# Kernel tuning notes

Hardware: AMD Instinct MI355X
Metric: run time of the kernel (lower is better)

Reference implementation:

```python
import jax, jax.numpy as jnp
from jax import lax
import numpy as np

B0 = 2          # batch
S = 32          # spatial grid side; L = S*S + 2
L = S * S + 2
DM = 256        # d_model
ED = 512        # d_inner = expand_factor * d_model
N = 16          # d_state
R = 16          # dt_rank = ceil(d_model/16)
K = 4           # d_conv


def _dwconv(x, w, b):
    # x: (B, L, ED) -> causal depthwise conv1d, kernel K, left-pad K-1 (== torch pad K-1 then [:, :, :L])
    xt = jnp.transpose(x, (0, 2, 1))  # (B, ED, L)
    o = lax.conv_general_dilated(xt, w, (1,), [(K - 1, 0)],
                                 feature_group_count=ED,
                                 dimension_numbers=('NCH', 'OIH', 'NCH'))
    return jnp.transpose(o + b[None, :, None], (0, 2, 1))


def _ssm(x, Alog, Dp, xp_w, dt_w, dt_b):
    # x: (B, L, ED); selective scan (mamba.py math, pscan=True path)
    A = -jnp.exp(Alog)                       # (ED, N)
    dBC = x @ xp_w.T                          # (B, L, R+2N)
    delta = jax.nn.softplus(dBC[..., :R] @ dt_w.T + dt_b)  # (B, L, ED)
    Bm = dBC[..., R:R + N]                    # (B, L, N)
    Cm = dBC[..., R + N:]                     # (B, L, N)
    dA = jnp.exp(delta[..., None] * A)        # (B, L, ED, N)
    dBx = (delta * x)[..., None] * Bm[:, :, None, :]  # (B, L, ED, N)

    def comb(e1, e2):
        a1, b1 = e1
        a2, b2 = e2
        return a1 * a2, a2 * b1 + b2

    _, hs = lax.associative_scan(comb, (dA, dBx), axis=1)  # h_t = dA_t*h_{t-1} + dBx_t
    return jnp.einsum('blen,bln->ble', hs, Cm) + Dp * x


def _cross(t):
    # keep first/last token, transpose the SxS interior grid (row-major <-> col-major)
    b, l, d = t.shape
    inner = t[:, 1:-1].reshape(b, S, S, d).transpose(0, 2, 1, 3).reshape(b, S * S, d)
    return jnp.concatenate([t[:, :1], inner, t[:, -1:]], axis=1)


def _branch(xz, cw, cb, xp, dw, db, Al, Dp):
    xa, za = jnp.split(xz, 2, axis=-1)
    xa = jax.nn.silu(_dwconv(xa, cw, cb))
    return _ssm(xa, Al, Dp, xp, dw, db) * jax.nn.silu(za)


def _forward(x, in_w, out_w, *p):
    xz = x @ in_w.T  # (B, L, 2*ED)
    (cwa, cba, xpa, dwa, dba, Ala, Da,
     cwb, cbb, xpb, dwb, dbb, Alb, Db,
     cwc, cbc, xpc, dwc, dbc, Alc, Dc,
     cwd, cbd, xpd, dwd, dbd, Ald, Dd) = p
    ga = _branch(xz, cwa, cba, xpa, dwa, dba, Ala, Da)                # forward scan
    gb = _branch(xz[:, ::-1], cwb, cbb, xpb, dwb, dbb, Alb, Db)       # reversed scan
    xzc = _cross(xz)
    gc = _branch(xzc, cwc, cbc, xpc, dwc, dbc, Alc, Dc)               # transposed scan
    gd = _branch(xzc[:, ::-1], cwd, cbd, xpd, dwd, dbd, Ald, Dd)      # reversed-transposed scan
    # gating commutes with token permutations, so reassemble gated outputs
    y = (ga + gb[:, ::-1] + _cross(gc) + _cross(gd)[:, ::-1]) * 0.25  # divide_output=True
    return y @ out_w.T


def setup_inputs() -> dict:
    keys = jax.random.split(jax.random.key(0), 64)
    it = iter(keys)

    def nrm(shape, scale=0.02):
        return scale * jax.random.normal(next(it), shape, dtype=jnp.float32)

    d = {}
    d['x'] = jax.random.normal(next(it), (B0, L, DM), dtype=jnp.float32)
    d['in_w'] = nrm((2 * ED, DM))
    d['out_w'] = nrm((DM, ED))
    std = R ** -0.5
    for s in ['a', 'b', 'c', 'd']:
        d[f'conv_w_{s}'] = nrm((ED, 1, K), 0.1)
        d[f'conv_b_{s}'] = jnp.zeros((ED,), jnp.float32)
        d[f'xp_w_{s}'] = nrm((R + 2 * N, ED))
        d[f'dt_w_{s}'] = jax.random.uniform(next(it), (ED, R), minval=-std, maxval=std, dtype=jnp.float32)
        dt = jnp.exp(jax.random.uniform(next(it), (ED,), dtype=jnp.float32)
                     * (np.float32(np.log(0.1)) - np.float32(np.log(0.001))) + np.float32(np.log(0.001)))
        d[f'dt_b_{s}'] = dt + jnp.log(-jnp.expm1(-dt))  # inverse-softplus init
        d[f'Alog_{s}'] = jnp.log(jnp.tile(jnp.arange(1, N + 1, dtype=jnp.float32), (ED, 1)))
        d[f'D_{s}'] = jnp.ones((ED,), jnp.float32)
    return d


def reference(x, in_w, out_w,
              conv_w_a, conv_b_a, xp_w_a, dt_w_a, dt_b_a, Alog_a, D_a,
              conv_w_b, conv_b_b, xp_w_b, dt_w_b, dt_b_b, Alog_b, D_b,
              conv_w_c, conv_b_c, xp_w_c, dt_w_c, dt_b_c, Alog_c, D_c,
              conv_w_d, conv_b_d, xp_w_d, dt_w_d, dt_b_d, Alog_d, D_d):
    return _forward(x, in_w, out_w,
                    conv_w_a, conv_b_a, xp_w_a, dt_w_a, dt_b_a, Alog_a, D_a,
                    conv_w_b, conv_b_b, xp_w_b, dt_w_b, dt_b_b, Alog_b, D_b,
                    conv_w_c, conv_b_c, xp_w_c, dt_w_c, dt_b_c, Alog_c, D_c,
                    conv_w_d, conv_b_d, xp_w_d, dt_w_d, dt_b_d, Alog_d, D_d)
```

## Files before the change

kernel.cpp:

```cpp
#include <hip/hip_runtime.h>
#include <math.h>

#define LL 1026
#define EDim 512
#define MM 2052
#define NC 16
#define LC 64

struct Params {
  const float* cw[4];
  const float* cb[4];
  const float* xpw[4];
  const float* dtw[4];
  const float* dtb[4];
  const float* Al[4];
  const float* Dp[4];
};

__device__ __forceinline__ int sigma_map(int branch, int l) {
  if (branch & 1) l = LL - 1 - l;
  if (branch & 2) {
    if (l > 0 && l < LL - 1) {
      int p = l - 1;
      l = 1 + ((p & 31) << 5) + (p >> 5);
    }
  }
  return l;
}

__device__ __forceinline__ float silu_f(float v) {
  return v * __builtin_amdgcn_rcpf(1.f + __expf(-v));
}
__device__ __forceinline__ float softplus_f(float s) {
  return fmaxf(s, 0.f) + __logf(1.f + __expf(-fabsf(s)));
}

template<int CTRL>
__device__ __forceinline__ float dpp_mov0(float x) {
  int r = __builtin_amdgcn_update_dpp(0, __float_as_int(x), CTRL, 0xF, 0xF, false);
  return __int_as_float(r);
}

__device__ __forceinline__ float red16(float r) {
  r += dpp_mov0<0xB1>(r);
  r += dpp_mov0<0x4E>(r);
  r += dpp_mov0<0x114>(r);
  r += dpp_mov0<0x118>(r);
  return r;
}

__global__ __launch_bounds__(256, 2) void k1_gemm_in(
    const float* __restrict__ x, const float* __restrict__ w,
    float* __restrict__ xa, float* __restrict__ sz) {
  __shared__ float As[32][68];
  __shared__ float Bs[32][68];
  const int t = threadIdx.x;
  const int tx = t & 15, ty = t >> 4;
  const int m0 = blockIdx.x * 64, n0 = blockIdx.y * 64;
  float acc[4][4] = {};
  for (int k0 = 0; k0 < 256; k0 += 32) {
    #pragma unroll
    for (int p = 0; p < 2; ++p) {
      int f = t + p * 256;
      int row = f >> 3, cf = f & 7;
      int gr = m0 + row; gr = gr < MM ? gr : MM - 1;
      float4 v = *(const float4*)(x + (size_t)gr * 256 + k0 + cf * 4);
      As[cf*4+0][row] = v.x; As[cf*4+1][row] = v.y;
      As[cf*4+2][row] = v.z; As[cf*4+3][row] = v.w;
      int gn = n0 + row;
      float4 u = *(const float4*)(w + (size_t)gn * 256 + k0 + cf * 4);
      Bs[cf*4+0][row] = u.x; Bs[cf*4+1][row] = u.y;
      Bs[cf*4+2][row] = u.z; Bs[cf*4+3][row] = u.w;
    }
    __syncthreads();
    #pragma unroll
    for (int k = 0; k < 32; ++k) {
      float4 av = *(const float4*)&As[k][ty*4];
      float4 bv = *(const float4*)&Bs[k][tx*4];
      float a0 = av.x, a1 = av.y, a2 = av.z, a3 = av.w;
      float b0 = bv.x, b1 = bv.y, b2 = bv.z, b3 = bv.w;
      acc[0][0]=fmaf(a0,b0,acc[0][0]); acc[0][1]=fmaf(a0,b1,acc[0][1]); acc[0][2]=fmaf(a0,b2,acc[0][2]); acc[0][3]=fmaf(a0,b3,acc[0][3]);
      acc[1][0]=fmaf(a1,b0,acc[1][0]); acc[1][1]=fmaf(a1,b1,acc[1][1]); acc[1][2]=fmaf(a1,b2,acc[1][2]); acc[1][3]=fmaf(a1,b3,acc[1][3]);
      acc[2][0]=fmaf(a2,b0,acc[2][0]); acc[2][1]=fmaf(a2,b1,acc[2][1]); acc[2][2]=fmaf(a2,b2,acc[2][2]); acc[2][3]=fmaf(a2,b3,acc[2][3]);
      acc[3][0]=fmaf(a3,b0,acc[3][0]); acc[3][1]=fmaf(a3,b1,acc[3][1]); acc[3][2]=fmaf(a3,b2,acc[3][2]); acc[3][3]=fmaf(a3,b3,acc[3][3]);
    }
    __syncthreads();
  }
  #pragma unroll
  for (int i = 0; i < 4; ++i) {
    int gm = m0 + ty*4 + i;
    if (gm < MM) {
      #pragma unroll
      for (int j = 0; j < 4; ++j) {
        int gn = n0 + tx*4 + j;
        float v = acc[i][j];
        if (gn < 512) xa[(size_t)gm*512 + gn] = v;
        else          sz[(size_t)gm*512 + gn - 512] = silu_f(v);
      }
    }
  }
}

__global__ __launch_bounds__(256, 4) void k2a_conv(
    Params P, const float* __restrict__ xa, float* __restrict__ xac,
    float* __restrict__ acc_out) {
  const int t = threadIdx.x;
  const int l0 = blockIdx.x * 8;
  const int b  = blockIdx.y;
  const int br = blockIdx.z;
  const int e0 = 2 * t;

  if (br == 0 && l0 < LL) {
    int nrow = LL - l0; if (nrow > 8) nrow = 8;
    float* ab = acc_out + ((size_t)b * LL + l0) * 512;
    for (int idx = t; idx < nrow * 512; idx += 256) ab[idx] = 0.f;
  }

  const float* cw = P.cw[br];
  const float w00 = cw[e0*4+0], w01 = cw[e0*4+1], w02 = cw[e0*4+2], w03 = cw[e0*4+3];
  const float w10 = cw[(e0+1)*4+0], w11 = cw[(e0+1)*4+1], w12 = cw[(e0+1)*4+2], w13 = cw[(e0+1)*4+3];
  const float cb0 = P.cb[br][e0], cb1 = P.cb[br][e0+1];
  const float* xab = xa + (size_t)b * LL * 512;
  float* xob = xac + ((size_t)(br*2 + b) * LL) * 512;

  float h0x=0,h0y=0,h1x=0,h1y=0,h2x=0,h2y=0,h3x=0,h3y=0;
  #pragma unroll
  for (int i = -3; i < 8; ++i) {
    int l = l0 + i;
    float cx = 0.f, cy = 0.f;
    if (l >= 0 && l < LL) {
      int pos = sigma_map(br, l);
      float2 v = *(const float2*)(xab + (size_t)pos * 512 + e0);
      cx = v.x; cy = v.y;
    }
    h0x=h1x; h0y=h1y; h1x=h2x; h1y=h2y; h2x=h3x; h2y=h3y; h3x=cx; h3y=cy;
    if (i >= 0 && l < LL) {
      float o0 = fmaf(w00,h0x, fmaf(w01,h1x, fmaf(w02,h2x, fmaf(w03,h3x, cb0))));
      float o1 = fmaf(w10,h0y, fmaf(w11,h1y, fmaf(w12,h2y, fmaf(w13,h3y, cb1))));
      *(float2*)(xob + (size_t)l * 512 + e0) = make_float2(silu_f(o0), silu_f(o1));
    }
  }
}

__global__ __launch_bounds__(256, 2) void k2b_proj(
    Params P, const float* __restrict__ xac,
    float* __restrict__ delta, float* __restrict__ bcg) {
  __shared__ float xcS[16][516];
  __shared__ float dBCs[16][49];
  const int t = threadIdx.x;
  const int l0 = blockIdx.x * 16;
  const int b  = blockIdx.y;
  const int br = blockIdx.z;
  const int e0 = 2 * t;
  const size_t obase = (size_t)(br*2 + b) * LL;

  #pragma unroll
  for (int p = 0; p < 8; ++p) {
    int idx = t + p*256;
    int row = idx >> 7, c4 = idx & 127;
    int l = l0 + row;
    float4 v = make_float4(0.f,0.f,0.f,0.f);
    if (l < LL) v = *(const float4*)(xac + (obase + l)*512 + c4*4);
    *(float4*)&xcS[row][c4*4] = v;
  }
  __syncthreads();

  const int rowi = t & 15;
  const int r0 = t >> 4;
  const float* xpw = P.xpw[br];
  const float4* xr4 = (const float4*)&xcS[rowi][0];
  const float4* wa = (const float4*)(xpw + (size_t)r0 * 512);
  const float4* wb = (const float4*)(xpw + (size_t)(r0 + 16) * 512);
  const float4* wc = (const float4*)(xpw + (size_t)(r0 + 32) * 512);
  float acc0 = 0.f, acc1 = 0.f, acc2 = 0.f;
  #pragma unroll 8
  for (int e4 = 0; e4 < 128; ++e4) {
    float4 xv = xr4[e4];
    float4 a = wa[e4], bb = wb[e4], c = wc[e4];
    acc0 = fmaf(xv.x,a.x, fmaf(xv.y,a.y, fmaf(xv.z,a.z, fmaf(xv.w,a.w, acc0))));
    acc1 = fmaf(xv.x,bb.x,fmaf(xv.y,bb.y,fmaf(xv.z,bb.z,fmaf(xv.w,bb.w,acc1))));
    acc2 = fmaf(xv.x,c.x, fmaf(xv.y,c.y, fmaf(xv.z,c.z, fmaf(xv.w,c.w, acc2))));
  }
  dBCs[rowi][r0]      = acc0;
  dBCs[rowi][r0 + 16] = acc1;
  dBCs[rowi][r0 + 32] = acc2;
  __syncthreads();

  for (int idx = t; idx < 512; idx += 256) {
    int row = idx >> 5, c = idx & 31;
    int l = l0 + row;
    if (l < LL) bcg[(obase + l)*32 + c] = dBCs[row][16 + c];
  }

  const float* dtw = P.dtw[br];
  float dw0[16], dw1[16];
  #pragma unroll
  for (int r = 0; r < 16; ++r) { dw0[r] = dtw[e0*16 + r]; dw1[r] = dtw[(e0+1)*16 + r]; }
  const float db0 = P.dtb[br][e0], db1 = P.dtb[br][e0+1];
  for (int row = 0; row < 16; ++row) {
    int l = l0 + row;
    if (l >= LL) break;
    float s0 = db0, s1 = db1;
    #pragma unroll
    for (int r = 0; r < 16; ++r) {
      float d = dBCs[row][r];
      s0 = fmaf(d, dw0[r], s0);
      s1 = fmaf(d, dw1[r], s1);
    }
    *(float2*)(delta + (obase + l)*512 + e0) = make_float2(softplus_f(s0), softplus_f(s1));
  }
}

__global__ __launch_bounds__(256, 4) void k3a_chunk(
    Params P, const float* __restrict__ xac, const float* __restrict__ delta,
    const float* __restrict__ bcg, float* __restrict__ Pc, float* __restrict__ Qc) {
  __shared__ float dT[16][36], xT[16][36], bT[16][36];
  const int t = threadIdx.x;
  const int eL = t >> 4, n = t & 15;
  const int e0 = blockIdx.x * 16;
  const int b = blockIdx.y;
  const int br = blockIdx.z / NC, c = blockIdx.z % NC;
  const size_t sbase = (size_t)(br*2 + b) * LL;
  const float* dl = delta + sbase * 512;
  const float* xc = xac + sbase * 512;
  const float* bc = bcg + sbase * 32;
  const float A_en = -__expf(P.Al[br][(e0 + eL)*16 + n]);
  const int l0 = c * LC;
  const int lend = (c == NC-1) ? LL : (l0 + LC);
  float h = 0.f, dsum = 0.f;

  for (int c0 = l0; c0 < lend; c0 += 32) {
    {
      const int idx = t & 127;
      const int s = idx >> 2, q = idx & 3;
      const int l = c0 + s;
      float4 v = make_float4(0.f,0.f,0.f,0.f);
      if (t < 128) {
        if (l < lend) v = *(const float4*)(dl + (size_t)l*512 + e0 + q*4);
        dT[q*4+0][s]=v.x; dT[q*4+1][s]=v.y; dT[q*4+2][s]=v.z; dT[q*4+3][s]=v.w;
        float4 u = make_float4(0.f,0.f,0.f,0.f);
        if (l < lend) u = *(const float4*)(bc + (size_t)l*32 + q*4);
        bT[q*4+0][s]=u.x; bT[q*4+1][s]=u.y; bT[q*4+2][s]=u.z; bT[q*4+3][s]=u.w;
      } else {
        if (l < lend) v = *(const float4*)(xc + (size_t)l*512 + e0 + q*4);
        xT[q*4+0][s]=v.x; xT[q*4+1][s]=v.y; xT[q*4+2][s]=v.z; xT[q*4+3][s]=v.w;
      }
    }
    __syncthreads();
    #pragma unroll
    for (int s4 = 0; s4 < 32; s4 += 4) {
      float4 dv = *(const float4*)&dT[eL][s4];
      float4 xv = *(const float4*)&xT[eL][s4];
      float4 bv = *(const float4*)&bT[n][s4];
      float g0 = __expf(dv.x*A_en), g1 = __expf(dv.y*A_en);
      float g2 = __expf(dv.z*A_en), g3 = __expf(dv.w*A_en);
      dsum += (dv.x+dv.y)+(dv.z+dv.w);
      h = fmaf(g0, h, dv.x*xv.x*bv.x);
      h = fmaf(g1, h, dv.y*xv.y*bv.y);
      h = fmaf(g2, h, dv.z*xv.z*bv.z);
      h = fmaf(g3, h, dv.w*xv.w*bv.w);
    }
    __syncthreads();
  }
  size_t oi = ((((size_t)(br*2 + b)*NC + c)*32 + blockIdx.x)*256 + t);
  Pc[oi] = __expf(dsum * A_en);
  Qc[oi] = h;
}

__global__ __launch_bounds__(256, 4) void k3b_scan(
    Params P, const float* __restrict__ xac, const float* __restrict__ delta,
    const float* __restrict__ bcg, const float* __restrict__ sz,
    const float* __restrict__ Pc, const float* __restrict__ Qc,
    float* __restrict__ acc_out) {
  __shared__ float dT[16][36], xT[16][36], bT[16][36], cT[16][36];
  __shared__ float yb[16][36];
  const int t = threadIdx.x;
  const int eL = t >> 4, n = t & 15;
  const int e0 = blockIdx.x * 16;
  const int b = blockIdx.y;
  const int br = blockIdx.z / NC, c = blockIdx.z % NC;
  const size_t sbase = (size_t)(br*2 + b) * LL;
  const float* dl = delta + sbase * 512;
  const float* xc = xac + sbase * 512;
  const float* bc = bcg + sbase * 32;
  const float A_en = -__expf(P.Al[br][(e0 + eL)*16 + n]);
  const float Dval = P.Dp[br][e0 + (t & 15)];
  const float* szb = sz + (size_t)b * LL * 512;
  float* ab = acc_out + (size_t)b * LL * 512;

  float h = 0.f;
  for (int cc = 0; cc < c; ++cc) {
    size_t ii = ((((size_t)(br*2 + b)*NC + cc)*32 + blockIdx.x)*256 + t);
    h = fmaf(Pc[ii], h, Qc[ii]);
  }

  const int l0c = c * LC;
  const int lend = (c == NC-1) ? LL : (l0c + LC);
  for (int c0 = l0c; c0 < lend; c0 += 32) {
    {
      const int idx = t & 127;
      const int s = idx >> 2, q = idx & 3;
      const int l = c0 + s;
      float4 v = make_float4(0.f,0.f,0.f,0.f);
      if (t < 128) {
        if (l < lend) v = *(const float4*)(dl + (size_t)l*512 + e0 + q*4);
        dT[q*4+0][s]=v.x; dT[q*4+1][s]=v.y; dT[q*4+2][s]=v.z; dT[q*4+3][s]=v.w;
      } else {
        if (l < lend) v = *(const float4*)(xc + (size_t)l*512 + e0 + q*4);
        xT[q*4+0][s]=v.x; xT[q*4+1][s]=v.y; xT[q*4+2][s]=v.z; xT[q*4+3][s]=v.w;
      }
    }
    {
      const int s = t >> 3, q = t & 7;
      const int l = c0 + s;
      float4 u = make_float4(0.f,0.f,0.f,0.f);
      if (l < lend) u = *(const float4*)(bc + (size_t)l*32 + q*4);
      if (q < 4) {
        bT[q*4+0][s]=u.x; bT[q*4+1][s]=u.y; bT[q*4+2][s]=u.z; bT[q*4+3][s]=u.w;
      } else {
        int q4 = (q-4)*4;
        cT[q4+0][s]=u.x; cT[q4+1][s]=u.y; cT[q4+2][s]=u.z; cT[q4+3][s]=u.w;
      }
    }
    __syncthreads();

    #pragma unroll
    for (int s4 = 0; s4 < 32; s4 += 4) {
      float4 dv = *(const float4*)&dT[eL][s4];
      float4 xv = *(const float4*)&xT[eL][s4];
      float4 bv = *(const float4*)&bT[n][s4];
      float4 cv = *(const float4*)&cT[n][s4];
      float r0, r1, r2, r3;
      h = fmaf(__expf(dv.x*A_en), h, dv.x*xv.x*bv.x); r0 = red16(h*cv.x);
      h = fmaf(__expf(dv.y*A_en), h, dv.y*xv.y*bv.y); r1 = red16(h*cv.y);
      h = fmaf(__expf(dv.z*A_en), h, dv.z*xv.z*bv.z); r2 = red16(h*cv.z);
      h = fmaf(__expf(dv.w*A_en), h, dv.w*xv.w*bv.w); r3 = red16(h*cv.w);
      if (n == 15) *(float4*)&yb[eL][s4] = make_float4(r0, r1, r2, r3);
    }
    __syncthreads();

    #pragma unroll
    for (int p = 0; p < 2; ++p) {
      int idx = t + p*256;
      int s = idx >> 4, ee = idx & 15;
      int l = c0 + s;
      if (l < lend) {
        float yv = fmaf(Dval, xT[ee][s], yb[ee][s]);
        int pos = sigma_map(br, l);
        float szv = szb[(size_t)pos * 512 + e0 + ee];
        atomicAdd(ab + (size_t)pos * 512 + e0 + ee, 0.25f * yv * szv);
      }
    }
    __syncthreads();
  }
}

__global__ __launch_bounds__(256, 2) void k4_gemm_out(
    const float* __restrict__ acc_in, const float* __restrict__ w,
    float* __restrict__ out) {
  __shared__ float As[32][38];
  __shared__ float Bs[32][38];
  const int t = threadIdx.x;
  const int tx = t & 15, ty = t >> 4;
  const int m0 = blockIdx.x * 32, n0 = blockIdx.y * 32;
  float acc[2][2] = {};
  for (int k0 = 0; k0 < 512; k0 += 32) {
    #pragma unroll
    for (int p = 0; p < 4; ++p) {
      int idx = t + p*256;
      int row = idx >> 5, kk = idx & 31;
      int gm = m0 + row; gm = gm < MM ? gm : MM - 1;
      As[kk][row] = acc_in[(size_t)gm*512 + k0 + kk];
    }
    #pragma unroll
    for (int p = 0; p < 4; ++p) {
      int idx = t + p*256;
      int row = idx >> 5, kk = idx & 31;
      Bs[kk][row] = w[(size_t)(n0 + row)*512 + k0 + kk];
    }
    __syncthreads();
    #pragma unroll
    for (int k = 0; k < 32; ++k) {
      float2 av = *(const float2*)&As[k][ty*2];
      float2 bv = *(const float2*)&Bs[k][tx*2];
      acc[0][0]=fmaf(av.x,bv.x,acc[0][0]); acc[0][1]=fmaf(av.x,bv.y,acc[0][1]);
      acc[1][0]=fmaf(av.y,bv.x,acc[1][0]); acc[1][1]=fmaf(av.y,bv.y,acc[1][1]);
    }
    __syncthreads();
  }
  #pragma unroll
  for (int i = 0; i < 2; ++i) {
    int gm = m0 + ty*2 + i;
    if (gm < MM) {
      #pragma unroll
      for (int j = 0; j < 2; ++j)
        out[(size_t)gm*256 + n0 + tx*2 + j] = acc[i][j];
    }
  }
}

extern "C" void kernel_launch(void* const* d_in, const int* in_sizes, int n_in,
                              void* d_out, int out_size, void* d_ws, size_t ws_size,
                              hipStream_t stream) {
  const float* x    = (const float*)d_in[0];
  const float* in_w = (const float*)d_in[1];
  const float* out_w= (const float*)d_in[2];
  Params prm;
  for (int s = 0; s < 4; ++s) {
    prm.cw[s]  = (const float*)d_in[3 + s*7 + 0];
    prm.cb[s]  = (const float*)d_in[3 + s*7 + 1];
    prm.xpw[s] = (const float*)d_in[3 + s*7 + 2];
    prm.dtw[s] = (const float*)d_in[3 + s*7 + 3];
    prm.dtb[s] = (const float*)d_in[3 + s*7 + 4];
    prm.Al[s]  = (const float*)d_in[3 + s*7 + 5];
    prm.Dp[s]  = (const float*)d_in[3 + s*7 + 6];
  }
  float* ws = (float*)d_ws;
  const size_t SZ1 = (size_t)MM * 512;
  float* xa   = ws;
  float* szp  = ws + SZ1;
  float* xac  = ws + 2*SZ1;
  float* dlt  = ws + 6*SZ1;
  float* bc   = ws + 10*SZ1;
  float* acc  = ws + 10*SZ1 + (size_t)4*MM*32;
  float* Pc   = acc + SZ1;
  float* Qc   = Pc + (size_t)8*NC*32*256;

  k1_gemm_in<<<dim3(33, 16), 256, 0, stream>>>(x, in_w, xa, szp);
  k2a_conv  <<<dim3(129, 2, 4), 256, 0, stream>>>(prm, xa, xac, acc);
  k2b_proj  <<<dim3(65, 2, 4), 256, 0, stream>>>(prm, xac, dlt, bc);
  k3a_chunk <<<dim3(32, 2, 4*NC), 256, 0, stream>>>(prm, xac, dlt, bc, Pc, Qc);
  k3b_scan  <<<dim3(32, 2, 4*NC), 256, 0, stream>>>(prm, xac, dlt, bc, szp, Pc, Qc, acc);
  k4_gemm_out<<<dim3(65, 8), 256, 0, stream>>>(acc, out_w, (float*)d_out);
}
```

Before: 281.2 us.

## Recompute delta inside scan kernels from low-rank dt projection instead of storing it

```diff
diff --git a/kernel.cpp b/kernel.cpp
--- a/kernel.cpp
+++ b/kernel.cpp
@@ -142,20 +142,19 @@
   }
 }
 
-__global__ __launch_bounds__(256, 2) void k2b_proj(
+__global__ __launch_bounds__(256, 4) void k2b_proj(
     Params P, const float* __restrict__ xac,
-    float* __restrict__ delta, float* __restrict__ bcg) {
-  __shared__ float xcS[16][516];
-  __shared__ float dBCs[16][49];
-  const int t = threadIdx.x;
-  const int l0 = blockIdx.x * 16;
+    float* __restrict__ dbc16, float* __restrict__ bcg) {
+  __shared__ float xcS[8][516];
+  __shared__ float dBCs[8][52];
+  const int t = threadIdx.x;
+  const int l0 = blockIdx.x * 8;
   const int b  = blockIdx.y;
   const int br = blockIdx.z;
-  const int e0 = 2 * t;
   const size_t obase = (size_t)(br*2 + b) * LL;
 
   #pragma unroll
-  for (int p = 0; p < 8; ++p) {
+  for (int p = 0; p < 4; ++p) {
     int idx = t + p*256;
     int row = idx >> 7, c4 = idx & 127;
     int l = l0 + row;
@@ -165,85 +164,105 @@
   }
   __syncthreads();
 
-  const int rowi = t & 15;
-  const int r0 = t >> 4;
+  const int rowi = t & 7;
+  const int rg = t >> 3;
   const float* xpw = P.xpw[br];
   const float4* xr4 = (const float4*)&xcS[rowi][0];
-  const float4* wa = (const float4*)(xpw + (size_t)r0 * 512);
-  const float4* wb = (const float4*)(xpw + (size_t)(r0 + 16) * 512);
-  const float4* wc = (const float4*)(xpw + (size_t)(r0 + 32) * 512);
-  float acc0 = 0.f, acc1 = 0.f, acc2 = 0.f;
-  #pragma unroll 8
-  for (int e4 = 0; e4 < 128; ++e4) {
-    float4 xv = xr4[e4];
-    float4 a = wa[e4], bb = wb[e4], c = wc[e4];
-    acc0 = fmaf(xv.x,a.x, fmaf(xv.y,a.y, fmaf(xv.z,a.z, fmaf(xv.w,a.w, acc0))));
-    acc1 = fmaf(xv.x,bb.x,fmaf(xv.y,bb.y,fmaf(xv.z,bb.z,fmaf(xv.w,bb.w,acc1))));
-    acc2 = fmaf(xv.x,c.x, fmaf(xv.y,c.y, fmaf(xv.z,c.z, fmaf(xv.w,c.w, acc2))));
-  }
-  dBCs[rowi][r0]      = acc0;
-  dBCs[rowi][r0 + 16] = acc1;
-  dBCs[rowi][r0 + 32] = acc2;
+  const float4* wa = (const float4*)(xpw + (size_t)rg * 512);
+  float acc0 = 0.f;
+  if (rg < 16) {
+    const float4* wb = (const float4*)(xpw + (size_t)(rg + 32) * 512);
+    float acc1 = 0.f;
+    #pragma unroll 8
+    for (int e4 = 0; e4 < 128; ++e4) {
+      float4 xv = xr4[e4];
+      float4 a = wa[e4], bb = wb[e4];
+      acc0 = fmaf(xv.x,a.x, fmaf(xv.y,a.y, fmaf(xv.z,a.z, fmaf(xv.w,a.w, acc0))));
+      acc1 = fmaf(xv.x,bb.x,fmaf(xv.y,bb.y,fmaf(xv.z,bb.z,fmaf(xv.w,bb.w,acc1))));
+    }
+    dBCs[rowi][rg]      = acc0;
+    dBCs[rowi][rg + 32] = acc1;
+  } else {
+    #pragma unroll 8
+    for (int e4 = 0; e4 < 128; ++e4) {
+      float4 xv = xr4[e4];
+      float4 a = wa[e4];
+      acc0 = fmaf(xv.x,a.x, fmaf(xv.y,a.y, fmaf(xv.z,a.z, fmaf(xv.w,a.w, acc0))));
+    }
+    dBCs[rowi][rg] = acc0;
+  }
   __syncthreads();
 
-  for (int idx = t; idx < 512; idx += 256) {
-    int row = idx >> 5, c = idx & 31;
+  if (t < 128) {
+    int row = t >> 4, r = t & 15;
+    int l = l0 + row;
+    if (l < LL) dbc16[(obase + l)*16 + r] = dBCs[row][r];
+  }
+  {
+    int row = t >> 5, c = t & 31;
     int l = l0 + row;
     if (l < LL) bcg[(obase + l)*32 + c] = dBCs[row][16 + c];
   }
-
-  const float* dtw = P.dtw[br];
-  float dw0[16], dw1[16];
-  #pragma unroll
-  for (int r = 0; r < 16; ++r) { dw0[r] = dtw[e0*16 + r]; dw1[r] = dtw[(e0+1)*16 + r]; }
-  const float db0 = P.dtb[br][e0], db1 = P.dtb[br][e0+1];
-  for (int row = 0; row < 16; ++row) {
-    int l = l0 + row;
-    if (l >= LL) break;
-    float s0 = db0, s1 = db1;
-    #pragma unroll
-    for (int r = 0; r < 16; ++r) {
-      float d = dBCs[row][r];
-      s0 = fmaf(d, dw0[r], s0);
-      s1 = fmaf(d, dw1[r], s1);
-    }
-    *(float2*)(delta + (obase + l)*512 + e0) = make_float2(softplus_f(s0), softplus_f(s1));
-  }
 }
 
 __global__ __launch_bounds__(256, 4) void k3a_chunk(
-    Params P, const float* __restrict__ xac, const float* __restrict__ delta,
+    Params P, const float* __restrict__ xac, const float* __restrict__ dbc16,
     const float* __restrict__ bcg, float* __restrict__ Pc, float* __restrict__ Qc) {
   __shared__ float dT[16][36], xT[16][36], bT[16][36];
+  __shared__ float rT[32][20];
+  __shared__ float dtwS[16][17];
+  __shared__ float dtbS[16];
   const int t = threadIdx.x;
   const int eL = t >> 4, n = t & 15;
   const int e0 = blockIdx.x * 16;
   const int b = blockIdx.y;
   const int br = blockIdx.z / NC, c = blockIdx.z % NC;
   const size_t sbase = (size_t)(br*2 + b) * LL;
-  const float* dl = delta + sbase * 512;
+  const float* rb = dbc16 + sbase * 16;
   const float* xc = xac + sbase * 512;
   const float* bc = bcg + sbase * 32;
   const float A_en = -__expf(P.Al[br][(e0 + eL)*16 + n]);
+  {
+    int ee = t >> 4, r = t & 15;
+    dtwS[ee][r] = P.dtw[br][(e0 + ee)*16 + r];
+    if (t < 16) dtbS[t] = P.dtb[br][e0 + t];
+  }
   const int l0 = c * LC;
   const int lend = (c == NC-1) ? LL : (l0 + LC);
   float h = 0.f, dsum = 0.f;
+  __syncthreads();
 
   for (int c0 = l0; c0 < lend; c0 += 32) {
     {
       const int idx = t & 127;
       const int s = idx >> 2, q = idx & 3;
       const int l = c0 + s;
-      float4 v = make_float4(0.f,0.f,0.f,0.f);
       if (t < 128) {
-        if (l < lend) v = *(const float4*)(dl + (size_t)l*512 + e0 + q*4);
-        dT[q*4+0][s]=v.x; dT[q*4+1][s]=v.y; dT[q*4+2][s]=v.z; dT[q*4+3][s]=v.w;
+        float4 v = make_float4(0.f,0.f,0.f,0.f);
+        if (l < lend) v = *(const float4*)(rb + (size_t)l*16 + q*4);
+        *(float4*)&rT[s][q*4] = v;
         float4 u = make_float4(0.f,0.f,0.f,0.f);
         if (l < lend) u = *(const float4*)(bc + (size_t)l*32 + q*4);
         bT[q*4+0][s]=u.x; bT[q*4+1][s]=u.y; bT[q*4+2][s]=u.z; bT[q*4+3][s]=u.w;
       } else {
+        float4 v = make_float4(0.f,0.f,0.f,0.f);
         if (l < lend) v = *(const float4*)(xc + (size_t)l*512 + e0 + q*4);
         xT[q*4+0][s]=v.x; xT[q*4+1][s]=v.y; xT[q*4+2][s]=v.z; xT[q*4+3][s]=v.w;
+      }
+    }
+    __syncthreads();
+    {
+      int ee = t & 15, s0 = t >> 4;
+      #pragma unroll
+      for (int ss = s0; ss < 32; ss += 16) {
+        float dv = 0.f;
+        if (c0 + ss < lend) {
+          float a = dtbS[ee];
+          #pragma unroll
+          for (int r = 0; r < 16; ++r) a = fmaf(rT[ss][r], dtwS[ee][r], a);
+          dv = softplus_f(a);
+        }
+        dT[ee][ss] = dv;
       }
     }
     __syncthreads();
@@ -268,31 +287,40 @@
 }
 
 __global__ __launch_bounds__(256, 4) void k3b_scan(
-    Params P, const float* __restrict__ xac, const float* __restrict__ delta,
+    Params P, const float* __restrict__ xac, const float* __restrict__ dbc16,
     const float* __restrict__ bcg, const float* __restrict__ sz,
     const float* __restrict__ Pc, const float* __restrict__ Qc,
     float* __restrict__ acc_out) {
   __shared__ float dT[16][36], xT[16][36], bT[16][36], cT[16][36];
   __shared__ float yb[16][36];
+  __shared__ float rT[32][20];
+  __shared__ float dtwS[16][17];
+  __shared__ float dtbS[16];
   const int t = threadIdx.x;
   const int eL = t >> 4, n = t & 15;
   const int e0 = blockIdx.x * 16;
   const int b = blockIdx.y;
   const int br = blockIdx.z / NC, c = blockIdx.z % NC;
   const size_t sbase = (size_t)(br*2 + b) * LL;
-  const float* dl = delta + sbase * 512;
+  const float* rb = dbc16 + sbase * 16;
   const float* xc = xac + sbase * 512;
   const float* bc = bcg + sbase * 32;
   const float A_en = -__expf(P.Al[br][(e0 + eL)*16 + n]);
   const float Dval = P.Dp[br][e0 + (t & 15)];
   const float* szb = sz + (size_t)b * LL * 512;
   float* ab = acc_out + (size_t)b * LL * 512;
+  {
+    int ee = t >> 4, r = t & 15;
+    dtwS[ee][r] = P.dtw[br][(e0 + ee)*16 + r];
+    if (t < 16) dtbS[t] = P.dtb[br][e0 + t];
+  }
 
   float h = 0.f;
   for (int cc = 0; cc < c; ++cc) {
     size_t ii = ((((size_t)(br*2 + b)*NC + cc)*32 + blockIdx.x)*256 + t);
     h = fmaf(Pc[ii], h, Qc[ii]);
   }
+  __syncthreads();
 
   const int l0c = c * LC;
   const int lend = (c == NC-1) ? LL : (l0c + LC);
@@ -301,11 +329,12 @@
       const int idx = t & 127;
       const int s = idx >> 2, q = idx & 3;
       const int l = c0 + s;
-      float4 v = make_float4(0.f,0.f,0.f,0.f);
       if (t < 128) {
-        if (l < lend) v = *(const float4*)(dl + (size_t)l*512 + e0 + q*4);
-        dT[q*4+0][s]=v.x; dT[q*4+1][s]=v.y; dT[q*4+2][s]=v.z; dT[q*4+3][s]=v.w;
+        float4 v = make_float4(0.f,0.f,0.f,0.f);
+        if (l < lend) v = *(const float4*)(rb + (size_t)l*16 + q*4);
+        *(float4*)&rT[s][q*4] = v;
       } else {
+        float4 v = make_float4(0.f,0.f,0.f,0.f);
         if (l < lend) v = *(const float4*)(xc + (size_t)l*512 + e0 + q*4);
         xT[q*4+0][s]=v.x; xT[q*4+1][s]=v.y; xT[q*4+2][s]=v.z; xT[q*4+3][s]=v.w;
       }
@@ -320,6 +349,21 @@
       } else {
         int q4 = (q-4)*4;
         cT[q4+0][s]=u.x; cT[q4+1][s]=u.y; cT[q4+2][s]=u.z; cT[q4+3][s]=u.w;
+      }
+    }
+    __syncthreads();
+    {
+      int ee = t & 15, s0 = t >> 4;
+      #pragma unroll
+      for (int ss = s0; ss < 32; ss += 16) {
+        float dv = 0.f;
+        if (c0 + ss < lend) {
+          float a = dtbS[ee];
+          #pragma unroll
+          for (int r = 0; r < 16; ++r) a = fmaf(rT[ss][r], dtwS[ee][r], a);
+          dv = softplus_f(a);
+        }
+        dT[ee][ss] = dv;
       }
     }
     __syncthreads();
@@ -417,19 +461,19 @@
   }
   float* ws = (float*)d_ws;
   const size_t SZ1 = (size_t)MM * 512;
-  float* xa   = ws;
-  float* szp  = ws + SZ1;
-  float* xac  = ws + 2*SZ1;
-  float* dlt  = ws + 6*SZ1;
-  float* bc   = ws + 10*SZ1;
-  float* acc  = ws + 10*SZ1 + (size_t)4*MM*32;
-  float* Pc   = acc + SZ1;
-  float* Qc   = Pc + (size_t)8*NC*32*256;
+  float* xa    = ws;
+  float* szp   = ws + SZ1;
+  float* xac   = ws + 2*SZ1;
+  float* bc    = ws + 6*SZ1;
+  float* acc   = bc + (size_t)4*MM*32;
+  float* Pc    = acc + SZ1;
+  float* Qc    = Pc + (size_t)8*NC*32*256;
+  float* dbc16 = Qc + (size_t)8*NC*32*256;
 
   k1_gemm_in<<<dim3(33, 16), 256, 0, stream>>>(x, in_w, xa, szp);
   k2a_conv  <<<dim3(129, 2, 4), 256, 0, stream>>>(prm, xa, xac, acc);
-  k2b_proj  <<<dim3(65, 2, 4), 256, 0, stream>>>(prm, xac, dlt, bc);
-  k3a_chunk <<<dim3(32, 2, 4*NC), 256, 0, stream>>>(prm, xac, dlt, bc, Pc, Qc);
-  k3b_scan  <<<dim3(32, 2, 4*NC), 256, 0, stream>>>(prm, xac, dlt, bc, szp, Pc, Qc, acc);
+  k2b_proj  <<<dim3(129, 2, 4), 256, 0, stream>>>(prm, xac, dbc16, bc);
+  k3a_chunk <<<dim3(32, 2, 4*NC), 256, 0, stream>>>(prm, xac, dbc16, bc, Pc, Qc);
+  k3b_scan  <<<dim3(32, 2, 4*NC), 256, 0, stream>>>(prm, xac, dbc16, bc, szp, Pc, Qc, acc);
   k4_gemm_out<<<dim3(65, 8), 256, 0, stream>>>(acc, out_w, (float*)d_out);
 }
```

Result: faster. 275.1 us (-2.2%).
